# Kernel optimization log

Measured on AMD Instinct MI355X. Metric: run time of the kernel, lower is better.

## Reference

```python
import jax, jax.numpy as jnp
import numpy as np

EPS = 1e-5
NUM_LAYERS = 3


def _batchnorm(h, g, b):
    mean = h.mean(axis=0)
    var = h.var(axis=0)  # biased variance, matches torch BatchNorm training math
    return (h - mean) * jax.lax.rsqrt(var + EPS) * g + b


def setup_inputs() -> dict:
    key = jax.random.key(0)
    ks = jax.random.split(key, 8)
    N, E, D, H, OUT = 100000, 1600000, 128, 128, 64
    s = 0.08  # weight scale for numerical sanity
    return {
        "x": jax.random.normal(ks[0], (N, D), jnp.float32),
        "edge_index": jax.random.randint(ks[1], (2, E), 0, N, jnp.int64),
        "Wl": jax.random.normal(ks[2], (NUM_LAYERS, D, H), jnp.float32) * s,
        "bl": jnp.zeros((NUM_LAYERS, H), jnp.float32),
        "Wr": jax.random.normal(ks[3], (NUM_LAYERS, D, H), jnp.float32) * s,
        "gamma": jnp.ones((NUM_LAYERS, H), jnp.float32),
        "beta": jnp.zeros((NUM_LAYERS, H), jnp.float32),
        "W1": jax.random.normal(ks[4], (D + NUM_LAYERS * H, 2 * OUT), jnp.float32) * s,
        "b1": jnp.zeros((2 * OUT,), jnp.float32),
        "g1": jnp.ones((2 * OUT,), jnp.float32),
        "be1": jnp.zeros((2 * OUT,), jnp.float32),
        "W2": jax.random.normal(ks[5], (2 * OUT, OUT), jnp.float32) * s,
        "b2": jnp.zeros((OUT,), jnp.float32),
    }


def reference(x, edge_index, Wl, bl, Wr, gamma, beta, W1, b1, g1, be1, W2, b2):
    # GraphSAGE: stacked SAGEConv(mean aggr) + BatchNorm + ReLU, JK-concat, 2-layer MLP head.
    # Dropout is identity (eval mode).
    N = x.shape[0]
    src, dst = edge_index[0], edge_index[1]
    deg = jax.ops.segment_sum(jnp.ones((src.shape[0],), x.dtype), dst, num_segments=N)
    inv_deg = (1.0 / jnp.maximum(deg, 1.0))[:, None]  # [N,1]
    xs = [x]
    h = x
    for i in range(NUM_LAYERS):
        # mean-aggregate neighbor features, then linear (same math as PyG SAGEConv)
        agg = jax.ops.segment_sum(h[src], dst, num_segments=N) * inv_deg  # [N,D]
        h = agg @ Wl[i] + bl[i] + h @ Wr[i]
        h = _batchnorm(h, gamma[i], beta[i])
        h = jax.nn.relu(h)
        xs.append(h)
    z = jnp.concatenate(xs, axis=-1)  # [N, D + L*H]
    z = _batchnorm(z @ W1 + b1, g1, be1)
    z = jax.nn.leaky_relu(z, negative_slope=0.01)
    return z @ W2 + b2
```

## Files before the change

kernel.cpp:

```cpp
#include <hip/hip_runtime.h>
#include <hip/hip_bf16.h>

#define CDIV(a,b) (((a)+(b)-1)/(b))

typedef __attribute__((ext_vector_type(8))) short short8_t;
typedef __attribute__((ext_vector_type(4))) float f32x4;

__device__ __forceinline__ float b2f(ushort u){
    union { uint i; float f; } v; v.i = ((uint)u) << 16; return v.f;
}
__device__ __forceinline__ ushort f2b(float f){
    __hip_bfloat16 h = __float2bfloat16(f);
    return *reinterpret_cast<ushort*>(&h);
}

__global__ __launch_bounds__(256) void k_bcount(
    const int* __restrict__ dst, int E, int nbuck, int* __restrict__ bcnt)
{
    __shared__ int cnt[512];
    const int t = threadIdx.x;
    for (int i = t; i < nbuck; i += 256) cnt[i] = 0;
    __syncthreads();
    const int e0 = blockIdx.x * 4096;
    #pragma unroll
    for (int q = 0; q < 16; ++q){
        int idx = e0 + q*256 + t;
        if (idx < E) atomicAdd(&cnt[dst[idx] >> 8], 1);
    }
    __syncthreads();
    for (int i = t; i < nbuck; i += 256){
        int c = cnt[i];
        if (c) atomicAdd(&bcnt[i], c);
    }
}

__global__ void k_bscan(const int* __restrict__ bcnt, int nbuck, int E,
                        int* __restrict__ bbase, int* __restrict__ gcur)
{
    __shared__ int s[512];
    int t = threadIdx.x;
    int v = (t < nbuck) ? bcnt[t] : 0;
    s[t] = v;
    __syncthreads();
    for (int off = 1; off < 512; off <<= 1){
        int x = (t >= off) ? s[t-off] : 0;
        __syncthreads();
        s[t] += x;
        __syncthreads();
    }
    if (t < nbuck){ int e = s[t] - v; bbase[t] = e; gcur[t] = e; }
    if (t == 0) bbase[nbuck] = E;
}

__global__ __launch_bounds__(256) void k_bucketA(
    const int* __restrict__ src, const int* __restrict__ dst, int E,
    int nbuck, int* __restrict__ gcur, uint* __restrict__ ebuf)
{
    __shared__ int cnt[512];
    __shared__ int base[512];
    const int t  = threadIdx.x;
    const int e0 = blockIdx.x * 4096;
    for (int i = t; i < nbuck; i += 256) cnt[i] = 0;
    __syncthreads();
    uint pk[16]; int mb[16];
    #pragma unroll
    for (int q = 0; q < 16; ++q){
        int idx = e0 + q*256 + t;
        int b = -1; uint pkv = 0;
        if (idx < E){
            int s = src[idx], d = dst[idx];
            b = d >> 8;
            pkv = (uint)s | ((uint)(d & 255) << 24);
            atomicAdd(&cnt[b], 1);
        }
        mb[q] = b; pk[q] = pkv;
    }
    __syncthreads();
    for (int i = t; i < nbuck; i += 256){
        int c = cnt[i];
        base[i] = c ? atomicAdd(&gcur[i], c) : 0;
    }
    __syncthreads();
    for (int i = t; i < nbuck; i += 256) cnt[i] = 0;
    __syncthreads();
    #pragma unroll
    for (int q = 0; q < 16; ++q){
        if (mb[q] >= 0){
            int b   = mb[q];
            int pos = base[b] + atomicAdd(&cnt[b], 1);
            ebuf[pos] = pk[q];
        }
    }
}

__global__ __launch_bounds__(256) void k_build(
    const uint* __restrict__ ebuf, const int* __restrict__ bbase,
    int N, int E, int* __restrict__ row_ptr, float* __restrict__ inv_deg,
    int* __restrict__ col_idx)
{
    __shared__ int cnt[256];
    __shared__ int scn[256];
    const int b = blockIdx.x;
    const int t = threadIdx.x;
    const int n0 = b << 8;
    const int ebase = bbase[b], eend = bbase[b+1];

    cnt[t] = 0;
    __syncthreads();
    for (int j = ebase + t; j < eend; j += 256)
        atomicAdd(&cnt[ebuf[j] >> 24], 1);
    __syncthreads();

    int d = cnt[t];
    scn[t] = d;
    __syncthreads();
    for (int off = 1; off < 256; off <<= 1){
        int x = (t >= off) ? scn[t-off] : 0;
        __syncthreads();
        scn[t] += x;
        __syncthreads();
    }
    int excl = scn[t] - d;
    int node = n0 + t;
    if (node < N){
        row_ptr[node] = ebase + excl;
        inv_deg[node] = 1.0f / (float)(d > 1 ? d : 1);
    }
    if (b == 0 && t == 0) row_ptr[N] = E;

    cnt[t] = excl;
    __syncthreads();
    for (int j = ebase + t; j < eend; j += 256){
        uint e = ebuf[j];
        int p = atomicAdd(&cnt[e >> 24], 1);
        col_idx[ebase + p] = (int)(e & 0xFFFFFFu);
    }
}

__global__ void k_cvt_x(const float* __restrict__ in, ushort* __restrict__ out, int n4){
    int i = blockIdx.x*blockDim.x + threadIdx.x;
    if (i >= n4) return;
    float4 v = reinterpret_cast<const float4*>(in)[i];
    ushort4 o; o.x=f2b(v.x); o.y=f2b(v.y); o.z=f2b(v.z); o.w=f2b(v.w);
    reinterpret_cast<ushort4*>(out)[i] = o;
}

__global__ void k_cvt_t(const float* __restrict__ in, ushort* __restrict__ out,
                        int K, int C, int total){
    int i = blockIdx.x*blockDim.x + threadIdx.x;
    if (i >= total) return;
    int kc = K*C;
    int s = i / kc, r = i - s*kc;
    int k = r / C, c = r - k*C;
    out[s*kc + c*K + k] = f2b(in[i]);
}

template<int NORM>
__global__ __launch_bounds__(256) void k_agg_bf(
    const ushort* __restrict__ h, const int* __restrict__ row_ptr,
    const int* __restrict__ col_idx, const float* __restrict__ inv_deg,
    const float* __restrict__ ssp, ushort* __restrict__ agg, int N)
{
    int node = (blockIdx.x*blockDim.x + threadIdx.x) >> 6;
    int lane = threadIdx.x & 63;
    if (node >= N) return;
    const int g = lane >> 4, l15 = lane & 15;
    const int beg = row_ptr[node], end = row_ptr[node+1];
    const size_t co = (size_t)l15 * 8;

    float scv[8], shv[8];
    if (NORM){
        float4 c0 = *reinterpret_cast<const float4*>(ssp + co);
        float4 c1 = *reinterpret_cast<const float4*>(ssp + co + 4);
        float4 s0 = *reinterpret_cast<const float4*>(ssp + 128 + co);
        float4 s1 = *reinterpret_cast<const float4*>(ssp + 128 + co + 4);
        scv[0]=c0.x; scv[1]=c0.y; scv[2]=c0.z; scv[3]=c0.w;
        scv[4]=c1.x; scv[5]=c1.y; scv[6]=c1.z; scv[7]=c1.w;
        shv[0]=s0.x; shv[1]=s0.y; shv[2]=s0.z; shv[3]=s0.w;
        shv[4]=s1.x; shv[5]=s1.y; shv[6]=s1.z; shv[7]=s1.w;
    }

    float2 a2[4];
    #pragma unroll
    for (int q = 0; q < 4; ++q) a2[q] = make_float2(0.f, 0.f);

    auto acc8 = [&](uint4 v){
        uint w[4] = {v.x, v.y, v.z, v.w};
        #pragma unroll
        for (int q = 0; q < 4; ++q){
            union { uint i; float f; } lo, hi;
            lo.i = w[q] << 16;
            hi.i = w[q] & 0xffff0000u;
            float fl = lo.f, fh = hi.f;
            if (NORM){
                fl = fmaxf(fl*scv[2*q]   + shv[2*q],   0.f);
                fh = fmaxf(fh*scv[2*q+1] + shv[2*q+1], 0.f);
            }
            a2[q].x += fl;
            a2[q].y += fh;
        }
    };

    int j = beg + g;
    while (j + 4 < end){
        int s0 = col_idx[j];
        int s1 = col_idx[j+4];
        uint4 v0 = *reinterpret_cast<const uint4*>(h + (size_t)s0*128 + co);
        uint4 v1 = *reinterpret_cast<const uint4*>(h + (size_t)s1*128 + co);
        acc8(v0); acc8(v1);
        j += 8;
    }
    if (j < end){
        int s0 = col_idx[j];
        uint4 v0 = *reinterpret_cast<const uint4*>(h + (size_t)s0*128 + co);
        acc8(v0);
    }

    #pragma unroll
    for (int q = 0; q < 4; ++q){
        a2[q].x += __shfl_xor(a2[q].x, 16);
        a2[q].y += __shfl_xor(a2[q].y, 16);
        a2[q].x += __shfl_xor(a2[q].x, 32);
        a2[q].y += __shfl_xor(a2[q].y, 32);
    }

    if (g == 0){
        float sc = inv_deg[node];
        uint r[4];
        #pragma unroll
        for (int q = 0; q < 4; ++q)
            r[q] = (uint)f2b(a2[q].x*sc) | ((uint)f2b(a2[q].y*sc) << 16);
        *reinterpret_cast<uint4*>(agg + (size_t)node*128 + co) =
            make_uint4(r[0], r[1], r[2], r[3]);
    }
}

__device__ __forceinline__ short8_t norm_frag(short8_t a, const float* __restrict__ sp,
                                              int kbase, int leaky)
{
    float4 c0 = *reinterpret_cast<const float4*>(sp + kbase);
    float4 c1 = *reinterpret_cast<const float4*>(sp + kbase + 4);
    float4 h0 = *reinterpret_cast<const float4*>(sp + 128 + kbase);
    float4 h1 = *reinterpret_cast<const float4*>(sp + 128 + kbase + 4);
    float cs[8] = {c0.x,c0.y,c0.z,c0.w,c1.x,c1.y,c1.z,c1.w};
    float hs[8] = {h0.x,h0.y,h0.z,h0.w,h1.x,h1.y,h1.z,h1.w};
    uint* au = reinterpret_cast<uint*>(&a);
    short8_t r;
    uint* ru = reinterpret_cast<uint*>(&r);
    #pragma unroll
    for (int q = 0; q < 4; ++q){
        float lo = b2f((ushort)(au[q] & 0xffffu));
        float hi = b2f((ushort)(au[q] >> 16));
        lo = lo*cs[2*q]   + hs[2*q];
        hi = hi*cs[2*q+1] + hs[2*q+1];
        if (leaky){ lo = lo > 0.f ? lo : 0.01f*lo; hi = hi > 0.f ? hi : 0.01f*hi; }
        else      { lo = fmaxf(lo, 0.f); hi = fmaxf(hi, 0.f); }
        ru[q] = (uint)f2b(lo) | ((uint)f2b(hi) << 16);
    }
    return r;
}

template<int NCF, int STATS, int OUTBF>
__global__ __launch_bounds__(256) void k_gemm_mfma(
    const ushort* __restrict__ A0, const ushort* __restrict__ T0,
    const ushort* __restrict__ A1, const ushort* __restrict__ T1,
    const ushort* __restrict__ A2, const ushort* __restrict__ T2,
    const ushort* __restrict__ A3, const ushort* __restrict__ T3,
    const float* __restrict__ ns0, const float* __restrict__ ns1,
    const float* __restrict__ ns2, const float* __restrict__ ns3,
    int m0, int m1, int m2, int m3,
    int P, const float* __restrict__ bias,
    ushort* __restrict__ out_bf, float* __restrict__ out_f32,
    float* __restrict__ partials, int N)
{
    __shared__ ushort Ws[NCF*16*128];
    const int t   = threadIdx.x;
    const int w   = t >> 6, l = t & 63;
    const int l15 = l & 15, lg = l >> 4;
    const int r0   = blockIdx.x * 128;
    const int wrow = w * 32;

    f32x4 acc[2][NCF];
    #pragma unroll
    for (int i = 0; i < 2; ++i)
        #pragma unroll
        for (int j = 0; j < NCF; ++j) acc[i][j] = (f32x4){0.f,0.f,0.f,0.f};

    for (int p = 0; p < P; ++p){
        const ushort* A  = (p==0)?A0:(p==1)?A1:(p==2)?A2:A3;
        const ushort* T  = (p==0)?T0:(p==1)?T1:(p==2)?T2:T3;
        const float*  ns = (p==0)?ns0:(p==1)?ns1:(p==2)?ns2:ns3;
        const int     md = (p==0)?m0:(p==1)?m1:(p==2)?m2:m3;
        if (p) __syncthreads();
        #pragma unroll
        for (int q = 0; q < NCF; ++q){
            int lin  = q*256 + t;
            int row  = lin >> 4, c16 = lin & 15;
            int c16s = c16 ^ (row & 7);
            uint4 v = *reinterpret_cast<const uint4*>(T + (size_t)row*128 + c16*8);
            *reinterpret_cast<uint4*>(&Ws[row*128 + c16s*8]) = v;
        }
        __syncthreads();
        #pragma unroll
        for (int kk = 0; kk < 4; ++kk){
            const int k0 = kk*32;
            short8_t a[2];
            #pragma unroll
            for (int rf = 0; rf < 2; ++rf){
                size_t gr = (size_t)(r0 + wrow + rf*16 + l15);
                a[rf] = *reinterpret_cast<const short8_t*>(A + gr*128 + k0 + lg*8);
            }
            if (md){
                a[0] = norm_frag(a[0], ns, k0 + lg*8, md == 2);
                a[1] = norm_frag(a[1], ns, k0 + lg*8, md == 2);
            }
            #pragma unroll
            for (int cf = 0; cf < NCF; ++cf){
                int row  = cf*16 + l15;
                int c16  = (k0 >> 3) + lg;
                int c16s = c16 ^ (row & 7);
                short8_t b = *reinterpret_cast<const short8_t*>(&Ws[row*128 + c16s*8]);
                acc[0][cf] = __builtin_amdgcn_mfma_f32_16x16x32_bf16(a[0], b, acc[0][cf], 0, 0, 0);
                acc[1][cf] = __builtin_amdgcn_mfma_f32_16x16x32_bf16(a[1], b, acc[1][cf], 0, 0, 0);
            }
        }
    }

    float bs[NCF];
    #pragma unroll
    for (int cf = 0; cf < NCF; ++cf) bs[cf] = bias[cf*16 + l15];

    float s1[NCF], s2[NCF];
    #pragma unroll
    for (int cf = 0; cf < NCF; ++cf){ s1[cf] = 0.f; s2[cf] = 0.f; }

    #pragma unroll
    for (int rf = 0; rf < 2; ++rf){
        #pragma unroll
        for (int q = 0; q < 4; ++q){
            int gr = r0 + wrow + rf*16 + lg*4 + q;
            bool valid = gr < N;
            #pragma unroll
            for (int cf = 0; cf < NCF; ++cf){
                float v = acc[rf][cf][q] + bs[cf];
                if (valid){
                    if (STATS){ s1[cf] += v; s2[cf] += v*v; }
                    int col = cf*16 + l15;
                    if (OUTBF) out_bf[(size_t)gr*(NCF*16) + col] = f2b(v);
                    else       out_f32[(size_t)gr*(NCF*16) + col] = v;
                }
            }
        }
    }
    if (STATS){
        #pragma unroll
        for (int cf = 0; cf < NCF; ++cf){
            s1[cf] += __shfl_xor(s1[cf], 16);
            s1[cf] += __shfl_xor(s1[cf], 32);
            s2[cf] += __shfl_xor(s2[cf], 16);
            s2[cf] += __shfl_xor(s2[cf], 32);
        }
        if (l < 16){
            float* pb = partials + (size_t)(blockIdx.x*4 + w)*256;
            #pragma unroll
            for (int cf = 0; cf < NCF; ++cf){
                pb[cf*16 + l15]       = s1[cf];
                pb[128 + cf*16 + l15] = s2[cf];
            }
        }
    }
}

__global__ void k_bnreduce(const float* __restrict__ partials, int I, int N,
                           const float* __restrict__ gamma, const float* __restrict__ beta,
                           float* __restrict__ ss)
{
    int c = blockIdx.x;
    int l = threadIdx.x;
    float s1 = 0.f, s2 = 0.f;
    for (int i = l; i < I; i += 64){
        s1 += partials[(size_t)i*256 + c];
        s2 += partials[(size_t)i*256 + 128 + c];
    }
    #pragma unroll
    for (int off = 32; off; off >>= 1){
        s1 += __shfl_xor(s1, off);
        s2 += __shfl_xor(s2, off);
    }
    if (l == 0){
        float m   = s1 / (float)N;
        float var = s2 / (float)N - m*m;
        float sc  = rsqrtf(var + 1e-5f) * gamma[c];
        ss[c]     = sc;
        ss[128+c] = beta[c] - m*sc;
    }
}

extern "C" void kernel_launch(void* const* d_in, const int* in_sizes, int n_in,
                              void* d_out, int out_size, void* d_ws, size_t ws_size,
                              hipStream_t stream)
{
    const float* x     = (const float*)d_in[0];
    const int*   ei    = (const int*)  d_in[1];
    const float* Wl    = (const float*)d_in[2];
    const float* bl    = (const float*)d_in[3];
    const float* Wr    = (const float*)d_in[4];
    const float* gamma = (const float*)d_in[5];
    const float* beta  = (const float*)d_in[6];
    const float* W1    = (const float*)d_in[7];
    const float* b1    = (const float*)d_in[8];
    const float* g1    = (const float*)d_in[9];
    const float* be1   = (const float*)d_in[10];
    const float* W2    = (const float*)d_in[11];
    const float* b2    = (const float*)d_in[12];
    float* out = (float*)d_out;

    const int N  = in_sizes[0] / 128;
    const int E  = in_sizes[1] / 2;
    const int NB = CDIV(N, 128);
    const size_t NPAD = (size_t)NB * 128;
    const int* src = ei;
    const int* dst = ei + E;

    const int NBUCK = CDIV(N, 256);

    char* w = (char*)d_ws;
    const size_t SB = NPAD * 128 * sizeof(ushort);
    ushort* x_bf = (ushort*)(w + 0*SB);
    ushort* pre0 = (ushort*)(w + 1*SB);
    ushort* pre1 = (ushort*)(w + 2*SB);
    ushort* pre2 = (ushort*)(w + 3*SB);
    ushort* aggb = (ushort*)(w + 4*SB);
    ushort* preh = (ushort*)(w + 5*SB);
    char* p = w + 6*SB;
    ushort* WtL = (ushort*)p;  p += (size_t)3*16384*2;
    ushort* WtR = (ushort*)p;  p += (size_t)3*16384*2;
    ushort* Wt1 = (ushort*)p;  p += (size_t)4*16384*2;
    ushort* Wt2 = (ushort*)p;  p += (size_t)8192*2;
    float* partials = (float*)p; p += (size_t)NB*4*256*sizeof(float);
    uint*  ebuf     = (uint*)p;  p += (size_t)E*4;
    int*   col_idx  = (int*)p;   p += (size_t)E*4;
    int*   row_ptr  = (int*)p;   p += (size_t)(N+1)*4;
    float* inv_deg  = (float*)p; p += (size_t)N*4;
    int*   bcnt     = (int*)p;   p += 512*4;
    int*   bbase    = (int*)p;   p += 516*4;
    int*   gcur     = (int*)p;   p += 512*4;
    float* ss0      = (float*)p; p += 256*4;
    float* ss1      = (float*)p; p += 256*4;
    float* ss2      = (float*)p; p += 256*4;
    float* ssh      = (float*)p; p += 256*4;

    const int n4 = N * 32;
    k_cvt_x<<<CDIV(n4,256), 256, 0, stream>>>(x, x_bf, n4);
    k_cvt_t<<<CDIV(3*16384,256), 256, 0, stream>>>(Wl, WtL, 128, 128, 3*16384);
    k_cvt_t<<<CDIV(3*16384,256), 256, 0, stream>>>(Wr, WtR, 128, 128, 3*16384);
    k_cvt_t<<<CDIV(4*16384,256), 256, 0, stream>>>(W1, Wt1, 128, 128, 4*16384);
    k_cvt_t<<<CDIV(8192,256),    256, 0, stream>>>(W2, Wt2, 128,  64, 8192);

    hipMemsetAsync(bcnt, 0, 512*4, stream);
    k_bcount<<<CDIV(E,4096), 256, 0, stream>>>(dst, E, NBUCK, bcnt);
    k_bscan<<<1, 512, 0, stream>>>(bcnt, NBUCK, E, bbase, gcur);
    k_bucketA<<<CDIV(E,4096), 256, 0, stream>>>(src, dst, E, NBUCK, gcur, ebuf);
    k_build<<<NBUCK, 256, 0, stream>>>(ebuf, bbase, N, E, row_ptr, inv_deg, col_idx);

    ushort* pre[3] = {pre0, pre1, pre2};
    float*  ssl[3] = {ss0, ss1, ss2};
    const int I = NB * 4;

    for (int L = 0; L < 3; ++L){
        if (L == 0)
            k_agg_bf<0><<<CDIV(N,4), 256, 0, stream>>>(x_bf, row_ptr, col_idx, inv_deg,
                                                       nullptr, aggb, N);
        else
            k_agg_bf<1><<<CDIV(N,4), 256, 0, stream>>>(pre[L-1], row_ptr, col_idx, inv_deg,
                                                       ssl[L-1], aggb, N);
        const ushort* hsrc = (L == 0) ? x_bf : pre[L-1];
        const float*  hns  = (L == 0) ? nullptr : ssl[L-1];
        int hmode = (L == 0) ? 0 : 1;
        k_gemm_mfma<8,1,1><<<NB, 256, 0, stream>>>(
            aggb, WtL + (size_t)L*16384,
            hsrc, WtR + (size_t)L*16384,
            nullptr, nullptr, nullptr, nullptr,
            nullptr, hns, nullptr, nullptr,
            0, hmode, 0, 0,
            2, bl + (size_t)L*128, pre[L], nullptr, partials, N);
        k_bnreduce<<<128, 64, 0, stream>>>(partials, I, N,
            gamma + (size_t)L*128, beta + (size_t)L*128, ssl[L]);
    }

    k_gemm_mfma<8,1,1><<<NB, 256, 0, stream>>>(
        x_bf, Wt1 + 0,
        pre0, Wt1 + 16384,
        pre1, Wt1 + 2*16384,
        pre2, Wt1 + 3*16384,
        nullptr, ss0, ss1, ss2,
        0, 1, 1, 1,
        4, b1, preh, nullptr, partials, N);
    k_bnreduce<<<128, 64, 0, stream>>>(partials, I, N, g1, be1, ssh);

    k_gemm_mfma<4,0,0><<<NB, 256, 0, stream>>>(
        preh, Wt2, nullptr, nullptr, nullptr, nullptr, nullptr, nullptr,
        ssh, nullptr, nullptr, nullptr,
        2, 0, 0, 0,
        1, b2, nullptr, out, partials, N);
}
```

Measured before the change: 491.4 us.

## Store node features in 16-column slices to localize gathers per slice

Node feature buffers change from row-major [N,128] to eight column slices of [NPAD,16]. The aggregation kernel now launches one block per 4 nodes per slice, each lane gathering 4 bytes per neighbor. The aim is to keep each slice's gather working set (about 3.2 MB) cache-resident while the slice is processed. The GEMM loads and stores, and the x conversion, are adapted to the sliced layout. The trade-off is eight times more aggregation blocks, col_idx being reread once per slice, and narrower 32-byte-per-row A-tile loads and strided bf16 stores in the GEMM.

```diff
diff --git a/kernel.cpp b/kernel.cpp
--- a/kernel.cpp
+++ b/kernel.cpp
@@ -137,12 +137,15 @@
     }
 }
 
-__global__ void k_cvt_x(const float* __restrict__ in, ushort* __restrict__ out, int n4){
+__global__ void k_cvt_x(const float* __restrict__ in, ushort* __restrict__ out,
+                        int n4, uint SS){
     int i = blockIdx.x*blockDim.x + threadIdx.x;
     if (i >= n4) return;
     float4 v = reinterpret_cast<const float4*>(in)[i];
+    uint row = (uint)(i >> 5);
+    uint c4  = (uint)(i & 31) * 4;
     ushort4 o; o.x=f2b(v.x); o.y=f2b(v.y); o.z=f2b(v.z); o.w=f2b(v.w);
-    reinterpret_cast<ushort4*>(out)[i] = o;
+    *reinterpret_cast<ushort4*>(out + (size_t)(c4 >> 4)*SS + row*16 + (c4 & 15)) = o;
 }
 
 __global__ void k_cvt_t(const float* __restrict__ in, ushort* __restrict__ out,
@@ -156,82 +159,61 @@
 }
 
 template<int NORM>
-__global__ __launch_bounds__(256) void k_agg_bf(
+__global__ __launch_bounds__(256) void k_agg_sl(
     const ushort* __restrict__ h, const int* __restrict__ row_ptr,
     const int* __restrict__ col_idx, const float* __restrict__ inv_deg,
-    const float* __restrict__ ssp, ushort* __restrict__ agg, int N)
-{
-    int node = (blockIdx.x*blockDim.x + threadIdx.x) >> 6;
-    int lane = threadIdx.x & 63;
+    const float* __restrict__ ssp, ushort* __restrict__ agg, int N, uint SS)
+{
+    const int slice = blockIdx.x & 7;
+    const int node  = (blockIdx.x >> 3) * 4 + (threadIdx.x >> 6);
     if (node >= N) return;
-    const int g = lane >> 4, l15 = lane & 15;
+    const int lane = threadIdx.x & 63;
+    const int g = lane >> 3, l8 = lane & 7;
     const int beg = row_ptr[node], end = row_ptr[node+1];
-    const size_t co = (size_t)l15 * 8;
-
-    float scv[8], shv[8];
+    const ushort* hs = h + (size_t)slice * SS;
+    const uint c0 = (uint)l8 * 2;
+
+    float sc0, sc1, sh0, sh1;
     if (NORM){
-        float4 c0 = *reinterpret_cast<const float4*>(ssp + co);
-        float4 c1 = *reinterpret_cast<const float4*>(ssp + co + 4);
-        float4 s0 = *reinterpret_cast<const float4*>(ssp + 128 + co);
-        float4 s1 = *reinterpret_cast<const float4*>(ssp + 128 + co + 4);
-        scv[0]=c0.x; scv[1]=c0.y; scv[2]=c0.z; scv[3]=c0.w;
-        scv[4]=c1.x; scv[5]=c1.y; scv[6]=c1.z; scv[7]=c1.w;
-        shv[0]=s0.x; shv[1]=s0.y; shv[2]=s0.z; shv[3]=s0.w;
-        shv[4]=s1.x; shv[5]=s1.y; shv[6]=s1.z; shv[7]=s1.w;
-    }
-
-    float2 a2[4];
-    #pragma unroll
-    for (int q = 0; q < 4; ++q) a2[q] = make_float2(0.f, 0.f);
-
-    auto acc8 = [&](uint4 v){
-        uint w[4] = {v.x, v.y, v.z, v.w};
-        #pragma unroll
-        for (int q = 0; q < 4; ++q){
-            union { uint i; float f; } lo, hi;
-            lo.i = w[q] << 16;
-            hi.i = w[q] & 0xffff0000u;
-            float fl = lo.f, fh = hi.f;
-            if (NORM){
-                fl = fmaxf(fl*scv[2*q]   + shv[2*q],   0.f);
-                fh = fmaxf(fh*scv[2*q+1] + shv[2*q+1], 0.f);
-            }
-            a2[q].x += fl;
-            a2[q].y += fh;
-        }
+        sc0 = ssp[slice*16 + c0];     sc1 = ssp[slice*16 + c0 + 1];
+        sh0 = ssp[128 + slice*16 + c0]; sh1 = ssp[128 + slice*16 + c0 + 1];
+    }
+
+    float a0 = 0.f, a1 = 0.f;
+    auto accv = [&](uint v){
+        union { uint i; float f; } lo, hi;
+        lo.i = v << 16;
+        hi.i = v & 0xffff0000u;
+        float fl = lo.f, fh = hi.f;
+        if (NORM){
+            fl = fmaxf(fl*sc0 + sh0, 0.f);
+            fh = fmaxf(fh*sc1 + sh1, 0.f);
+        }
+        a0 += fl; a1 += fh;
     };
 
     int j = beg + g;
-    while (j + 4 < end){
-        int s0 = col_idx[j];
-        int s1 = col_idx[j+4];
-        uint4 v0 = *reinterpret_cast<const uint4*>(h + (size_t)s0*128 + co);
-        uint4 v1 = *reinterpret_cast<const uint4*>(h + (size_t)s1*128 + co);
-        acc8(v0); acc8(v1);
-        j += 8;
+    while (j + 8 < end){
+        uint o0 = (uint)col_idx[j]   * 16u + c0;
+        uint o1 = (uint)col_idx[j+8] * 16u + c0;
+        uint v0 = *reinterpret_cast<const uint*>(hs + o0);
+        uint v1 = *reinterpret_cast<const uint*>(hs + o1);
+        accv(v0); accv(v1);
+        j += 16;
     }
     if (j < end){
-        int s0 = col_idx[j];
-        uint4 v0 = *reinterpret_cast<const uint4*>(h + (size_t)s0*128 + co);
-        acc8(v0);
-    }
-
-    #pragma unroll
-    for (int q = 0; q < 4; ++q){
-        a2[q].x += __shfl_xor(a2[q].x, 16);
-        a2[q].y += __shfl_xor(a2[q].y, 16);
-        a2[q].x += __shfl_xor(a2[q].x, 32);
-        a2[q].y += __shfl_xor(a2[q].y, 32);
-    }
+        uint o0 = (uint)col_idx[j] * 16u + c0;
+        accv(*reinterpret_cast<const uint*>(hs + o0));
+    }
+
+    a0 += __shfl_xor(a0, 8);  a1 += __shfl_xor(a1, 8);
+    a0 += __shfl_xor(a0, 16); a1 += __shfl_xor(a1, 16);
+    a0 += __shfl_xor(a0, 32); a1 += __shfl_xor(a1, 32);
 
     if (g == 0){
         float sc = inv_deg[node];
-        uint r[4];
-        #pragma unroll
-        for (int q = 0; q < 4; ++q)
-            r[q] = (uint)f2b(a2[q].x*sc) | ((uint)f2b(a2[q].y*sc) << 16);
-        *reinterpret_cast<uint4*>(agg + (size_t)node*128 + co) =
-            make_uint4(r[0], r[1], r[2], r[3]);
+        uint r = (uint)f2b(a0*sc) | ((uint)f2b(a1*sc) << 16);
+        *reinterpret_cast<uint*>(agg + (size_t)slice*SS + (uint)node*16u + c0) = r;
     }
 }
 
@@ -271,7 +253,7 @@
     int m0, int m1, int m2, int m3,
     int P, const float* __restrict__ bias,
     ushort* __restrict__ out_bf, float* __restrict__ out_f32,
-    float* __restrict__ partials, int N)
+    float* __restrict__ partials, int N, uint SS)
 {
     __shared__ ushort Ws[NCF*16*128];
     const int t   = threadIdx.x;
@@ -304,15 +286,17 @@
         #pragma unroll
         for (int kk = 0; kk < 4; ++kk){
             const int k0 = kk*32;
+            const int kcol = k0 + lg*8;
+            const ushort* As = A + (size_t)(kcol >> 4)*SS + (kcol & 15);
             short8_t a[2];
             #pragma unroll
             for (int rf = 0; rf < 2; ++rf){
-                size_t gr = (size_t)(r0 + wrow + rf*16 + l15);
-                a[rf] = *reinterpret_cast<const short8_t*>(A + gr*128 + k0 + lg*8);
+                uint gr = (uint)(r0 + wrow + rf*16 + l15);
+                a[rf] = *reinterpret_cast<const short8_t*>(As + gr*16u);
             }
             if (md){
-                a[0] = norm_frag(a[0], ns, k0 + lg*8, md == 2);
-                a[1] = norm_frag(a[1], ns, k0 + lg*8, md == 2);
+                a[0] = norm_frag(a[0], ns, kcol, md == 2);
+                a[1] = norm_frag(a[1], ns, kcol, md == 2);
             }
             #pragma unroll
             for (int cf = 0; cf < NCF; ++cf){
@@ -345,9 +329,8 @@
                 float v = acc[rf][cf][q] + bs[cf];
                 if (valid){
                     if (STATS){ s1[cf] += v; s2[cf] += v*v; }
-                    int col = cf*16 + l15;
-                    if (OUTBF) out_bf[(size_t)gr*(NCF*16) + col] = f2b(v);
-                    else       out_f32[(size_t)gr*(NCF*16) + col] = v;
+                    if (OUTBF) out_bf[(size_t)cf*SS + (uint)gr*16u + l15] = f2b(v);
+                    else       out_f32[(size_t)gr*(NCF*16) + cf*16 + l15] = v;
                 }
             }
         }
@@ -419,6 +402,7 @@
     const int E  = in_sizes[1] / 2;
     const int NB = CDIV(N, 128);
     const size_t NPAD = (size_t)NB * 128;
+    const uint SS = (uint)(NPAD * 16);
     const int* src = ei;
     const int* dst = ei + E;
 
@@ -451,7 +435,7 @@
     float* ssh      = (float*)p; p += 256*4;
 
     const int n4 = N * 32;
-    k_cvt_x<<<CDIV(n4,256), 256, 0, stream>>>(x, x_bf, n4);
+    k_cvt_x<<<CDIV(n4,256), 256, 0, stream>>>(x, x_bf, n4, SS);
     k_cvt_t<<<CDIV(3*16384,256), 256, 0, stream>>>(Wl, WtL, 128, 128, 3*16384);
     k_cvt_t<<<CDIV(3*16384,256), 256, 0, stream>>>(Wr, WtR, 128, 128, 3*16384);
     k_cvt_t<<<CDIV(4*16384,256), 256, 0, stream>>>(W1, Wt1, 128, 128, 4*16384);
@@ -466,14 +450,15 @@
     ushort* pre[3] = {pre0, pre1, pre2};
     float*  ssl[3] = {ss0, ss1, ss2};
     const int I = NB * 4;
+    const int AGG_GRID = CDIV(N,4) * 8;
 
     for (int L = 0; L < 3; ++L){
         if (L == 0)
-            k_agg_bf<0><<<CDIV(N,4), 256, 0, stream>>>(x_bf, row_ptr, col_idx, inv_deg,
-                                                       nullptr, aggb, N);
+            k_agg_sl<0><<<AGG_GRID, 256, 0, stream>>>(x_bf, row_ptr, col_idx, inv_deg,
+                                                      nullptr, aggb, N, SS);
         else
-            k_agg_bf<1><<<CDIV(N,4), 256, 0, stream>>>(pre[L-1], row_ptr, col_idx, inv_deg,
-                                                       ssl[L-1], aggb, N);
+            k_agg_sl<1><<<AGG_GRID, 256, 0, stream>>>(pre[L-1], row_ptr, col_idx, inv_deg,
+                                                      ssl[L-1], aggb, N, SS);
         const ushort* hsrc = (L == 0) ? x_bf : pre[L-1];
         const float*  hns  = (L == 0) ? nullptr : ssl[L-1];
         int hmode = (L == 0) ? 0 : 1;
@@ -483,7 +468,7 @@
             nullptr, nullptr, nullptr, nullptr,
             nullptr, hns, nullptr, nullptr,
             0, hmode, 0, 0,
-            2, bl + (size_t)L*128, pre[L], nullptr, partials, N);
+            2, bl + (size_t)L*128, pre[L], nullptr, partials, N, SS);
         k_bnreduce<<<128, 64, 0, stream>>>(partials, I, N,
             gamma + (size_t)L*128, beta + (size_t)L*128, ssl[L]);
     }
@@ -495,12 +480,12 @@
         pre2, Wt1 + 3*16384,
         nullptr, ss0, ss1, ss2,
         0, 1, 1, 1,
-        4, b1, preh, nullptr, partials, N);
+        4, b1, preh, nullptr, partials, N, SS);
     k_bnreduce<<<128, 64, 0, stream>>>(partials, I, N, g1, be1, ssh);
 
     k_gemm_mfma<4,0,0><<<NB, 256, 0, stream>>>(
         preh, Wt2, nullptr, nullptr, nullptr, nullptr, nullptr, nullptr,
         ssh, nullptr, nullptr, nullptr,
         2, 0, 0, 0,
-        1, b2, nullptr, out, partials, N);
-}
+        1, b2, nullptr, out, partials, N, SS);
+}
```

Measured after the change: 911.6 us. 1.86x slower.

## Store GEMM activations in 16-column slab layout with row-major copies for gather

Applied to the files above, without the earlier changes.

Activations consumed by the MFMA GEMM are now stored in a column-slab layout (16 columns per slab, rows contiguous within a slab), so each lane's A-fragment load reads contiguous 32-byte rows inside a slab. The gather-based aggregation still needs row-major rows, so the x conversion and the first two layer GEMMs also write a row-major copy. The goal is more coalesced A loads and epilogue stores in the GEMMs. The cost is extra memory, duplicate writes of the activations, and per-element scattered stores in the epilogue.

```diff
diff --git a/kernel.cpp b/kernel.cpp
--- a/kernel.cpp
+++ b/kernel.cpp
@@ -137,12 +137,16 @@
     }
 }
 
-__global__ void k_cvt_x(const float* __restrict__ in, ushort* __restrict__ out, int n4){
+__global__ void k_cvt_x(const float* __restrict__ in, ushort* __restrict__ out_sl,
+                        ushort* __restrict__ out_rm, int n4, uint SS){
     int i = blockIdx.x*blockDim.x + threadIdx.x;
     if (i >= n4) return;
     float4 v = reinterpret_cast<const float4*>(in)[i];
+    uint row = (uint)(i >> 5);
+    uint c4  = (uint)(i & 31) * 4;
     ushort4 o; o.x=f2b(v.x); o.y=f2b(v.y); o.z=f2b(v.z); o.w=f2b(v.w);
-    reinterpret_cast<ushort4*>(out)[i] = o;
+    reinterpret_cast<ushort4*>(out_rm)[i] = o;
+    *reinterpret_cast<ushort4*>(out_sl + (size_t)(c4 >> 4)*SS + row*16 + (c4 & 15)) = o;
 }
 
 __global__ void k_cvt_t(const float* __restrict__ in, ushort* __restrict__ out,
@@ -159,7 +163,7 @@
 __global__ __launch_bounds__(256) void k_agg_bf(
     const ushort* __restrict__ h, const int* __restrict__ row_ptr,
     const int* __restrict__ col_idx, const float* __restrict__ inv_deg,
-    const float* __restrict__ ssp, ushort* __restrict__ agg, int N)
+    const float* __restrict__ ssp, ushort* __restrict__ agg, int N, uint SS)
 {
     int node = (blockIdx.x*blockDim.x + threadIdx.x) >> 6;
     int lane = threadIdx.x & 63;
@@ -230,8 +234,8 @@
         #pragma unroll
         for (int q = 0; q < 4; ++q)
             r[q] = (uint)f2b(a2[q].x*sc) | ((uint)f2b(a2[q].y*sc) << 16);
-        *reinterpret_cast<uint4*>(agg + (size_t)node*128 + co) =
-            make_uint4(r[0], r[1], r[2], r[3]);
+        ushort* dstp = agg + (size_t)(l15 >> 1)*SS + (uint)node*16u + (uint)(l15 & 1)*8;
+        *reinterpret_cast<uint4*>(dstp) = make_uint4(r[0], r[1], r[2], r[3]);
     }
 }
 
@@ -260,7 +264,7 @@
     return r;
 }
 
-template<int NCF, int STATS, int OUTBF>
+template<int NCF, int STATS, int OUTBF, int DUAL>
 __global__ __launch_bounds__(256) void k_gemm_mfma(
     const ushort* __restrict__ A0, const ushort* __restrict__ T0,
     const ushort* __restrict__ A1, const ushort* __restrict__ T1,
@@ -270,8 +274,9 @@
     const float* __restrict__ ns2, const float* __restrict__ ns3,
     int m0, int m1, int m2, int m3,
     int P, const float* __restrict__ bias,
-    ushort* __restrict__ out_bf, float* __restrict__ out_f32,
-    float* __restrict__ partials, int N)
+    ushort* __restrict__ out_bf, ushort* __restrict__ out_rm,
+    float* __restrict__ out_f32,
+    float* __restrict__ partials, int N, uint SS)
 {
     __shared__ ushort Ws[NCF*16*128];
     const int t   = threadIdx.x;
@@ -304,15 +309,17 @@
         #pragma unroll
         for (int kk = 0; kk < 4; ++kk){
             const int k0 = kk*32;
+            const int kcol = k0 + lg*8;
+            const ushort* As = A + (size_t)(kcol >> 4)*SS + (kcol & 15);
             short8_t a[2];
             #pragma unroll
             for (int rf = 0; rf < 2; ++rf){
-                size_t gr = (size_t)(r0 + wrow + rf*16 + l15);
-                a[rf] = *reinterpret_cast<const short8_t*>(A + gr*128 + k0 + lg*8);
+                uint gr = (uint)(r0 + wrow + rf*16 + l15);
+                a[rf] = *reinterpret_cast<const short8_t*>(As + gr*16u);
             }
             if (md){
-                a[0] = norm_frag(a[0], ns, k0 + lg*8, md == 2);
-                a[1] = norm_frag(a[1], ns, k0 + lg*8, md == 2);
+                a[0] = norm_frag(a[0], ns, kcol, md == 2);
+                a[1] = norm_frag(a[1], ns, kcol, md == 2);
             }
             #pragma unroll
             for (int cf = 0; cf < NCF; ++cf){
@@ -345,9 +352,13 @@
                 float v = acc[rf][cf][q] + bs[cf];
                 if (valid){
                     if (STATS){ s1[cf] += v; s2[cf] += v*v; }
-                    int col = cf*16 + l15;
-                    if (OUTBF) out_bf[(size_t)gr*(NCF*16) + col] = f2b(v);
-                    else       out_f32[(size_t)gr*(NCF*16) + col] = v;
+                    if (OUTBF){
+                        ushort hv = f2b(v);
+                        out_bf[(size_t)cf*SS + (uint)gr*16u + l15] = hv;
+                        if (DUAL) out_rm[(size_t)gr*128 + cf*16 + l15] = hv;
+                    } else {
+                        out_f32[(size_t)gr*(NCF*16) + cf*16 + l15] = v;
+                    }
                 }
             }
         }
@@ -419,6 +430,7 @@
     const int E  = in_sizes[1] / 2;
     const int NB = CDIV(N, 128);
     const size_t NPAD = (size_t)NB * 128;
+    const uint SS = (uint)(NPAD * 16);
     const int* src = ei;
     const int* dst = ei + E;
 
@@ -432,7 +444,10 @@
     ushort* pre2 = (ushort*)(w + 3*SB);
     ushort* aggb = (ushort*)(w + 4*SB);
     ushort* preh = (ushort*)(w + 5*SB);
-    char* p = w + 6*SB;
+    ushort* x_rm = (ushort*)(w + 6*SB);
+    ushort* prm0 = (ushort*)(w + 7*SB);
+    ushort* prm1 = (ushort*)(w + 8*SB);
+    char* p = w + 9*SB;
     ushort* WtL = (ushort*)p;  p += (size_t)3*16384*2;
     ushort* WtR = (ushort*)p;  p += (size_t)3*16384*2;
     ushort* Wt1 = (ushort*)p;  p += (size_t)4*16384*2;
@@ -451,7 +466,7 @@
     float* ssh      = (float*)p; p += 256*4;
 
     const int n4 = N * 32;
-    k_cvt_x<<<CDIV(n4,256), 256, 0, stream>>>(x, x_bf, n4);
+    k_cvt_x<<<CDIV(n4,256), 256, 0, stream>>>(x, x_bf, x_rm, n4, SS);
     k_cvt_t<<<CDIV(3*16384,256), 256, 0, stream>>>(Wl, WtL, 128, 128, 3*16384);
     k_cvt_t<<<CDIV(3*16384,256), 256, 0, stream>>>(Wr, WtR, 128, 128, 3*16384);
     k_cvt_t<<<CDIV(4*16384,256), 256, 0, stream>>>(W1, Wt1, 128, 128, 4*16384);
@@ -464,43 +479,53 @@
     k_build<<<NBUCK, 256, 0, stream>>>(ebuf, bbase, N, E, row_ptr, inv_deg, col_idx);
 
     ushort* pre[3] = {pre0, pre1, pre2};
+    ushort* prm[2] = {prm0, prm1};
     float*  ssl[3] = {ss0, ss1, ss2};
     const int I = NB * 4;
 
     for (int L = 0; L < 3; ++L){
         if (L == 0)
-            k_agg_bf<0><<<CDIV(N,4), 256, 0, stream>>>(x_bf, row_ptr, col_idx, inv_deg,
-                                                       nullptr, aggb, N);
+            k_agg_bf<0><<<CDIV(N,4), 256, 0, stream>>>(x_rm, row_ptr, col_idx, inv_deg,
+                                                       nullptr, aggb, N, SS);
         else
-            k_agg_bf<1><<<CDIV(N,4), 256, 0, stream>>>(pre[L-1], row_ptr, col_idx, inv_deg,
-                                                       ssl[L-1], aggb, N);
+            k_agg_bf<1><<<CDIV(N,4), 256, 0, stream>>>(prm[L-1], row_ptr, col_idx, inv_deg,
+                                                       ssl[L-1], aggb, N, SS);
         const ushort* hsrc = (L == 0) ? x_bf : pre[L-1];
         const float*  hns  = (L == 0) ? nullptr : ssl[L-1];
         int hmode = (L == 0) ? 0 : 1;
-        k_gemm_mfma<8,1,1><<<NB, 256, 0, stream>>>(
-            aggb, WtL + (size_t)L*16384,
-            hsrc, WtR + (size_t)L*16384,
-            nullptr, nullptr, nullptr, nullptr,
-            nullptr, hns, nullptr, nullptr,
-            0, hmode, 0, 0,
-            2, bl + (size_t)L*128, pre[L], nullptr, partials, N);
+        if (L < 2)
+            k_gemm_mfma<8,1,1,1><<<NB, 256, 0, stream>>>(
+                aggb, WtL + (size_t)L*16384,
+                hsrc, WtR + (size_t)L*16384,
+                nullptr, nullptr, nullptr, nullptr,
+                nullptr, hns, nullptr, nullptr,
+                0, hmode, 0, 0,
+                2, bl + (size_t)L*128, pre[L], prm[L], nullptr, partials, N, SS);
+        else
+            k_gemm_mfma<8,1,1,0><<<NB, 256, 0, stream>>>(
+                aggb, WtL + (size_t)L*16384,
+                hsrc, WtR + (size_t)L*16384,
+                nullptr, nullptr, nullptr, nullptr,
+                nullptr, hns, nullptr, nullptr,
+                0, hmode, 0, 0,
+                2, bl + (size_t)L*128, pre[L], nullptr, nullptr, partials, N, SS);
         k_bnreduce<<<128, 64, 0, stream>>>(partials, I, N,
             gamma + (size_t)L*128, beta + (size_t)L*128, ssl[L]);
     }
 
-    k_gemm_mfma<8,1,1><<<NB, 256, 0, stream>>>(
+    k_gemm_mfma<8,1,1,0><<<NB, 256, 0, stream>>>(
         x_bf, Wt1 + 0,
         pre0, Wt1 + 16384,
         pre1, Wt1 + 2*16384,
         pre2, Wt1 + 3*16384,
         nullptr, ss0, ss1, ss2,
         0, 1, 1, 1,
-        4, b1, preh, nullptr, partials, N);
+        4, b1, preh, nullptr, nullptr, partials, N, SS);
     k_bnreduce<<<128, 64, 0, stream>>>(partials, I, N, g1, be1, ssh);
 
-    k_gemm_mfma<4,0,0><<<NB, 256, 0, stream>>>(
+    k_gemm_mfma<4,0,0,0><<<NB, 256, 0, stream>>>(
         preh, Wt2, nullptr, nullptr, nullptr, nullptr, nullptr, nullptr,
         ssh, nullptr, nullptr, nullptr,
         2, 0, 0, 0,
-        1, b2, nullptr, out, partials, N);
-}
+        1, b2, nullptr, nullptr, out, partials, N, SS);
+}
```

New measurement: 510.1 us. 3.8% more time.

## Stage GEMM epilogue through LDS for coalesced stores; merge weight-convert kernels

Applied to the files above, without the earlier changes.

The GEMM epilogue now writes accumulator tiles into padded shared memory, then each thread stores 16-byte vectors of full rows, replacing scattered 2-byte or 4-byte strided global stores with coalesced ones. The shared buffer is enlarged to a fixed padded size to hold a 128-row output tile, which raises LDS use per block and may lower occupancy. Separately, four weight transpose-convert launches are merged into one kernel to cut launch overhead.

```diff
diff --git a/kernel.cpp b/kernel.cpp
--- a/kernel.cpp
+++ b/kernel.cpp
@@ -145,14 +145,34 @@
     reinterpret_cast<ushort4*>(out)[i] = o;
 }
 
-__global__ void k_cvt_t(const float* __restrict__ in, ushort* __restrict__ out,
-                        int K, int C, int total){
+__global__ void k_cvt_w(const float* __restrict__ Wl, const float* __restrict__ Wr,
+                        const float* __restrict__ W1, const float* __restrict__ W2,
+                        ushort* __restrict__ WtL, ushort* __restrict__ WtR,
+                        ushort* __restrict__ Wt1, ushort* __restrict__ Wt2)
+{
     int i = blockIdx.x*blockDim.x + threadIdx.x;
-    if (i >= total) return;
-    int kc = K*C;
-    int s = i / kc, r = i - s*kc;
-    int k = r / C, c = r - k*C;
-    out[s*kc + c*K + k] = f2b(in[i]);
+    const int S = 16384;
+    if (i < 3*S){
+        int s = i / S, r = i - s*S;
+        int k = r >> 7, c = r & 127;
+        WtL[s*S + c*128 + k] = f2b(Wl[i]);
+    } else if (i < 6*S){
+        i -= 3*S;
+        int s = i / S, r = i - s*S;
+        int k = r >> 7, c = r & 127;
+        WtR[s*S + c*128 + k] = f2b(Wr[i]);
+    } else if (i < 10*S){
+        i -= 6*S;
+        int s = i / S, r = i - s*S;
+        int k = r >> 7, c = r & 127;
+        Wt1[s*S + c*128 + k] = f2b(W1[i]);
+    } else {
+        i -= 10*S;
+        if (i < 8192){
+            int k = i >> 6, c = i & 63;
+            Wt2[c*128 + k] = f2b(W2[i]);
+        }
+    }
 }
 
 template<int NORM>
@@ -273,7 +293,7 @@
     ushort* __restrict__ out_bf, float* __restrict__ out_f32,
     float* __restrict__ partials, int N)
 {
-    __shared__ ushort Ws[NCF*16*128];
+    __shared__ ushort Ws[17920];
     const int t   = threadIdx.x;
     const int w   = t >> 6, l = t & 63;
     const int l15 = l & 15, lg = l >> 4;
@@ -334,24 +354,42 @@
     #pragma unroll
     for (int cf = 0; cf < NCF; ++cf){ s1[cf] = 0.f; s2[cf] = 0.f; }
 
+    __syncthreads();
+
     #pragma unroll
     for (int rf = 0; rf < 2; ++rf){
         #pragma unroll
         for (int q = 0; q < 4; ++q){
-            int gr = r0 + wrow + rf*16 + lg*4 + q;
-            bool valid = gr < N;
+            int row_l = wrow + rf*16 + lg*4 + q;
+            bool valid = (r0 + row_l) < N;
             #pragma unroll
             for (int cf = 0; cf < NCF; ++cf){
                 float v = acc[rf][cf][q] + bs[cf];
-                if (valid){
-                    if (STATS){ s1[cf] += v; s2[cf] += v*v; }
-                    int col = cf*16 + l15;
-                    if (OUTBF) out_bf[(size_t)gr*(NCF*16) + col] = f2b(v);
-                    else       out_f32[(size_t)gr*(NCF*16) + col] = v;
-                }
-            }
-        }
-    }
+                if (STATS && valid){ s1[cf] += v; s2[cf] += v*v; }
+                if (OUTBF) Ws[row_l*140 + cf*16 + l15] = f2b(v);
+                else       reinterpret_cast<float*>(Ws)[row_l*70 + cf*16 + l15] = v;
+            }
+        }
+    }
+    __syncthreads();
+
+    const int tr = t >> 4, tc = t & 15;
+    #pragma unroll
+    for (int i = 0; i < 8; ++i){
+        int row_l = i*16 + tr;
+        int gr = r0 + row_l;
+        if (gr < N){
+            if (OUTBF){
+                uint4 v = *reinterpret_cast<const uint4*>(&Ws[row_l*140 + tc*8]);
+                *reinterpret_cast<uint4*>(&out_bf[(size_t)gr*(NCF*16) + tc*8]) = v;
+            } else {
+                float4 v = *reinterpret_cast<const float4*>(
+                    &reinterpret_cast<float*>(Ws)[row_l*70 + tc*4]);
+                *reinterpret_cast<float4*>(&out_f32[(size_t)gr*(NCF*16) + tc*4]) = v;
+            }
+        }
+    }
+
     if (STATS){
         #pragma unroll
         for (int cf = 0; cf < NCF; ++cf){
@@ -452,10 +490,7 @@
 
     const int n4 = N * 32;
     k_cvt_x<<<CDIV(n4,256), 256, 0, stream>>>(x, x_bf, n4);
-    k_cvt_t<<<CDIV(3*16384,256), 256, 0, stream>>>(Wl, WtL, 128, 128, 3*16384);
-    k_cvt_t<<<CDIV(3*16384,256), 256, 0, stream>>>(Wr, WtR, 128, 128, 3*16384);
-    k_cvt_t<<<CDIV(4*16384,256), 256, 0, stream>>>(W1, Wt1, 128, 128, 4*16384);
-    k_cvt_t<<<CDIV(8192,256),    256, 0, stream>>>(W2, Wt2, 128,  64, 8192);
+    k_cvt_w<<<CDIV(10*16384+8192,256), 256, 0, stream>>>(Wl, Wr, W1, W2, WtL, WtR, Wt1, Wt2);
 
     hipMemsetAsync(bcnt, 0, 512*4, stream);
     k_bcount<<<CDIV(E,4096), 256, 0, stream>>>(dst, E, NBUCK, bcnt);
```

Measured after the change: 481.1 us. 1.02x faster.
